# Performance work log

Hardware: AMD Instinct MI355X
Metric: run time of the kernel (lower is better)

## Reference

```python
import jax, jax.numpy as jnp
import numpy as np

EPS = 1e-6
TAU = 0.07


def setup_inputs() -> dict:
    key = jax.random.key(0)
    kx, ky = jax.random.split(key)
    B, D = 4096, 1024
    x = jax.random.normal(kx, (B, D), dtype=jnp.float32)
    y = jax.random.normal(ky, (B, D), dtype=jnp.float32)
    return {"x": x, "y": y}


def reference(x, y):
    B = x.shape[0]
    # torch CosineSimilarity: dot / (max(||x||, eps) * max(||y||, eps))
    xn = x / jnp.maximum(jnp.linalg.norm(x, axis=-1, keepdims=True), EPS)
    yn = y / jnp.maximum(jnp.linalg.norm(y, axis=-1, keepdims=True), EPS)
    S = jnp.einsum('id,jd->ij', xn, yn)          # [B, B] cosine sims, S[i,j]=cos(x_i,y_j)
    E = jnp.exp(S / TAU)                          # bounded: |S|<=1 so exp <= e^{1/0.07}
    diag = jnp.diagonal(E)
    # original: sum_j (exp + eps) + eps  ->  sum_j exp + B*eps + eps
    extra = B * EPS + EPS
    row_denom = jnp.sum(E, axis=1) + extra        # x->y direction (loop 1)
    col_denom = jnp.sum(E, axis=0) + extra        # y->x direction (loop 2)
    coef = -1.0 / (2.0 * B)
    loss = coef * (jnp.sum(jnp.log(diag / row_denom)) + jnp.sum(jnp.log(diag / col_denom)))
    return loss
```

## Files before the change

### kernel.cpp

```cpp
#include <hip/hip_runtime.h>
#include <hip/hip_bf16.h>

#define NB 4096
#define DK 1024
#define EPSF 1e-6f
#define QSCALE 16.0f

typedef __attribute__((ext_vector_type(8))) int   i32x8_t;
typedef __attribute__((ext_vector_type(4))) int   i32x4_t;
typedef __attribute__((ext_vector_type(4))) float f32x4_t;


__device__ __forceinline__ void async16(const void* g, void* lds) {
    __builtin_amdgcn_global_load_lds(
        (const __attribute__((address_space(1))) void*)g,
        (__attribute__((address_space(3))) void*)lds, 16, 0, 0);
}

__global__ __launch_bounds__(256) void normalize_rows(
    const float* __restrict__ x, const float* __restrict__ y,
    unsigned char* __restrict__ xq, unsigned char* __restrict__ yq,
    float* __restrict__ sdiag, float* __restrict__ zerobuf)
{
    const int t = threadIdx.x;
    const int gid = blockIdx.x * 256 + t;
    if (gid < 2 * NB) zerobuf[gid] = 0.f;

    const int wave = t >> 6;
    const int lane = t & 63;
    const int row  = blockIdx.x * 4 + wave;

    const float4* xr = reinterpret_cast<const float4*>(x + (size_t)row * DK);
    const float4* yr = reinterpret_cast<const float4*>(y + (size_t)row * DK);

    float4 xv[4], yv[4];
    float ssx = 0.f, ssy = 0.f, sxy = 0.f;
    #pragma unroll
    for (int jj = 0; jj < 4; ++jj) {
        xv[jj] = xr[lane * 4 + jj];
        yv[jj] = yr[lane * 4 + jj];
        ssx += xv[jj].x*xv[jj].x + xv[jj].y*xv[jj].y + xv[jj].z*xv[jj].z + xv[jj].w*xv[jj].w;
        ssy += yv[jj].x*yv[jj].x + yv[jj].y*yv[jj].y + yv[jj].z*yv[jj].z + yv[jj].w*yv[jj].w;
        sxy += xv[jj].x*yv[jj].x + xv[jj].y*yv[jj].y + xv[jj].z*yv[jj].z + xv[jj].w*yv[jj].w;
    }
    #pragma unroll
    for (int off = 1; off < 64; off <<= 1) {
        ssx += __shfl_xor(ssx, off, 64);
        ssy += __shfl_xor(ssy, off, 64);
        sxy += __shfl_xor(sxy, off, 64);
    }
    const float invx = 1.0f / fmaxf(sqrtf(ssx), EPSF);
    const float invy = 1.0f / fmaxf(sqrtf(ssy), EPSF);
    const float sx = invx * QSCALE;
    const float sy = invy * QSCALE;

    i32x4_t xb, yb;
    #pragma unroll
    for (int jj = 0; jj < 4; ++jj) {
        int px = __builtin_amdgcn_cvt_pk_fp8_f32(xv[jj].x * sx, xv[jj].y * sx, 0, false);
        px     = __builtin_amdgcn_cvt_pk_fp8_f32(xv[jj].z * sx, xv[jj].w * sx, px, true);
        int py = __builtin_amdgcn_cvt_pk_fp8_f32(yv[jj].x * sy, yv[jj].y * sy, 0, false);
        py     = __builtin_amdgcn_cvt_pk_fp8_f32(yv[jj].z * sy, yv[jj].w * sy, py, true);
        xb[jj] = px;
        yb[jj] = py;
    }

    const int p = row >> 4, r = row & 15;
    const unsigned off = (unsigned)(p * 32 + (lane >> 3) * 4) * 512
                       + r * 128 + ((((lane & 7) ^ (r & 7))) << 4);
    *reinterpret_cast<i32x4_t*>(xq + off) = xb;
    *reinterpret_cast<i32x4_t*>(yq + off) = yb;

    if (lane == 0) sdiag[row] = sxy * invx * invy;
}

__global__ __launch_bounds__(512) void gemm_exp_sums(
    const unsigned char* __restrict__ xq, const unsigned char* __restrict__ yq,
    float* __restrict__ rowsum, float* __restrict__ colsum)
{
    __shared__ __align__(16) unsigned char As[32 * 1024];
    __shared__ __align__(16) unsigned char Bs[32 * 1024];

    const int t    = threadIdx.x;
    const int lane = t & 63;
    const int wave = t >> 6;
    const int q    = lane >> 4;
    const int l15  = lane & 15;

    const int R0 = blockIdx.y * 256;
    const int C0 = blockIdx.x * 256;
    const int wRow = (wave >> 2) * 64;
    const int wCol = (wave & 3) * 64;

    f32x4_t acc[2][4][4];
    #pragma unroll
    for (int hh = 0; hh < 2; hh++)
        #pragma unroll
        for (int i = 0; i < 4; i++)
            #pragma unroll
            for (int j = 0; j < 4; j++)
                acc[hh][i][j] = (f32x4_t){0.f, 0.f, 0.f, 0.f};

    const unsigned char* srcA =
        xq + (size_t)((R0 >> 4) + wave) * 16384 + lane * 16;
    const unsigned char* srcB =
        yq + (size_t)((C0 >> 4) + wave) * 16384 + lane * 16;

    const int sLo = (((2 * q)    ) ^ (l15 & 7)) << 4;
    const int sHi = (((2 * q) + 1) ^ (l15 & 7)) << 4;

    #pragma unroll 1
    for (int kb = 0; kb < 8; ++kb) {
        __syncthreads();
        #pragma unroll
        for (int h2 = 0; h2 < 2; ++h2) {
            async16(srcA + kb * 2048 + h2 * 1024,          &As[wave * 2048 + h2 * 1024]);
            async16(srcA + kb * 2048 + h2 * 1024 + 131072, &As[(wave + 8) * 2048 + h2 * 1024]);
            async16(srcB + kb * 2048 + h2 * 1024,          &Bs[wave * 2048 + h2 * 1024]);
            async16(srcB + kb * 2048 + h2 * 1024 + 131072, &Bs[(wave + 8) * 2048 + h2 * 1024]);
        }
        __syncthreads();

        i32x8_t bfr[4];
        #pragma unroll
        for (int nt = 0; nt < 4; ++nt) {
            const unsigned char* c = &Bs[((wCol >> 4) + nt) * 2048 + l15 * 128];
            const i32x4_t lo = *reinterpret_cast<const i32x4_t*>(c + sLo);
            const i32x4_t hi = *reinterpret_cast<const i32x4_t*>(c + sHi);
            bfr[nt][0] = lo[0]; bfr[nt][1] = lo[1]; bfr[nt][2] = lo[2]; bfr[nt][3] = lo[3];
            bfr[nt][4] = hi[0]; bfr[nt][5] = hi[1]; bfr[nt][6] = hi[2]; bfr[nt][7] = hi[3];
        }
        #pragma unroll
        for (int hh = 0; hh < 2; ++hh) {
            #pragma unroll
            for (int mt = 0; mt < 4; ++mt) {
                const unsigned char* c =
                    &As[((wRow >> 4) + hh * 8 + mt) * 2048 + l15 * 128];
                const i32x4_t lo = *reinterpret_cast<const i32x4_t*>(c + sLo);
                const i32x4_t hi = *reinterpret_cast<const i32x4_t*>(c + sHi);
                i32x8_t af;
                af[0] = lo[0]; af[1] = lo[1]; af[2] = lo[2]; af[3] = lo[3];
                af[4] = hi[0]; af[5] = hi[1]; af[6] = hi[2]; af[7] = hi[3];
                #pragma unroll
                for (int nt = 0; nt < 4; ++nt)
                    acc[hh][mt][nt] = __builtin_amdgcn_mfma_scale_f32_16x16x128_f8f6f4(
                        af, bfr[nt], acc[hh][mt][nt],
                        0, 0,
                        0, 0x7F7F7F7F,
                        0, 0x7F7F7F7F);
            }
        }
    }

    const float kScale = (float)(1.0 / (256.0 * 0.07 * 0.6931471805599453));
    float csum[4] = {0.f, 0.f, 0.f, 0.f};
    #pragma unroll
    for (int hh = 0; hh < 2; ++hh) {
        #pragma unroll
        for (int mt = 0; mt < 4; ++mt) {
            float rsum[4] = {0.f, 0.f, 0.f, 0.f};
            #pragma unroll
            for (int nt = 0; nt < 4; ++nt) {
                #pragma unroll
                for (int r = 0; r < 4; ++r) {
                    const float e = exp2f(acc[hh][mt][nt][r] * kScale);
                    rsum[r]  += e;
                    csum[nt] += e;
                }
            }
            #pragma unroll
            for (int r = 0; r < 4; ++r) {
                float v = rsum[r];
                v += __shfl_xor(v, 1, 64);
                v += __shfl_xor(v, 2, 64);
                v += __shfl_xor(v, 4, 64);
                v += __shfl_xor(v, 8, 64);
                if (l15 == 0)
                    atomicAdd(&rowsum[R0 + wRow + hh * 128 + mt * 16 + q * 4 + r], v);
            }
        }
    }
    #pragma unroll
    for (int nt = 0; nt < 4; ++nt) {
        float v = csum[nt];
        v += __shfl_xor(v, 16, 64);
        v += __shfl_xor(v, 32, 64);
        if (lane < 16)
            atomicAdd(&colsum[C0 + wCol + nt * 16 + l15], v);
    }
}

__global__ __launch_bounds__(1024) void finalize(
    const float* __restrict__ rowsum, const float* __restrict__ colsum,
    const float* __restrict__ sdiag, float* __restrict__ out)
{
    const float extra = (float)(NB * 1e-6 + 1e-6);
    double local = 0.0;
    for (int i = threadIdx.x; i < NB; i += 1024) {
        local += (double)sdiag[i] * (2.0 / 0.07)
               - (double)logf(rowsum[i] + extra)
               - (double)logf(colsum[i] + extra);
    }
    #pragma unroll
    for (int off = 1; off < 64; off <<= 1)
        local += __shfl_xor(local, off, 64);
    __shared__ double dred[16];
    const int wave = threadIdx.x >> 6;
    if ((threadIdx.x & 63) == 0) dred[wave] = local;
    __syncthreads();
    if (threadIdx.x == 0) {
        double tot = 0.0;
        #pragma unroll
        for (int w = 0; w < 16; ++w) tot += dred[w];
        out[0] = (float)(tot * (-1.0 / (2.0 * NB)));
    }
}

extern "C" void kernel_launch(void* const* d_in, const int* in_sizes, int n_in,
                              void* d_out, int out_size, void* d_ws, size_t ws_size,
                              hipStream_t stream)
{
    const float* x = (const float*)d_in[0];
    const float* y = (const float*)d_in[1];
    float* out = (float*)d_out;

    char* ws = (char*)d_ws;
    unsigned char* xq = (unsigned char*)ws;
    unsigned char* yq = (unsigned char*)(ws + (size_t)4 * 1024 * 1024);
    float* rowsum = (float*)(ws + (size_t)8 * 1024 * 1024);
    float* colsum = rowsum + NB;
    float* sdiag  = colsum + NB;

    normalize_rows<<<NB / 4, 256, 0, stream>>>(x, y, xq, yq, sdiag, rowsum);

    dim3 grid(16, 16);
    gemm_exp_sums<<<grid, 512, 0, stream>>>(xq, yq, rowsum, colsum);

    finalize<<<1, 1024, 0, stream>>>(rowsum, colsum, sdiag, out);
}
```

Measured before the change: 107.4 us.

## Shrink GEMM tile to 128x128 and double-buffer LDS with async prefetch

The fused FP8 GEMM+exp kernel moves from 256x256 tiles with 512 threads to 128x128 tiles with 256 threads, so the grid grows from 256 to 1024 blocks. It also double-buffers shared memory, prefetching the next K slab with async global-to-LDS loads while the MFMAs run on the current one, synchronised by waitcnt and barriers. The aim is to fill all CUs better and hide load latency. In exchange, each tile reuses less data, so global traffic and atomic row/column updates go up.

```diff
diff --git a/kernel.cpp b/kernel.cpp
--- a/kernel.cpp
+++ b/kernel.cpp
@@ -74,12 +74,11 @@
     if (lane == 0) sdiag[row] = sxy * invx * invy;
 }
 
-__global__ __launch_bounds__(512) void gemm_exp_sums(
+__global__ __launch_bounds__(256) void gemm_exp_sums(
     const unsigned char* __restrict__ xq, const unsigned char* __restrict__ yq,
     float* __restrict__ rowsum, float* __restrict__ colsum)
 {
-    __shared__ __align__(16) unsigned char As[32 * 1024];
-    __shared__ __align__(16) unsigned char Bs[32 * 1024];
+    __shared__ __align__(16) unsigned char LDS[2][32768];
 
     const int t    = threadIdx.x;
     const int lane = t & 63;
@@ -87,97 +86,108 @@
     const int q    = lane >> 4;
     const int l15  = lane & 15;
 
-    const int R0 = blockIdx.y * 256;
-    const int C0 = blockIdx.x * 256;
-    const int wRow = (wave >> 2) * 64;
-    const int wCol = (wave & 3) * 64;
-
-    f32x4_t acc[2][4][4];
-    #pragma unroll
-    for (int hh = 0; hh < 2; hh++)
-        #pragma unroll
-        for (int i = 0; i < 4; i++)
-            #pragma unroll
-            for (int j = 0; j < 4; j++)
-                acc[hh][i][j] = (f32x4_t){0.f, 0.f, 0.f, 0.f};
+    const int R0 = blockIdx.y * 128;
+    const int C0 = blockIdx.x * 128;
+    const int wRow = (wave >> 1) * 64;
+    const int wCol = (wave & 1) * 64;
+
+    f32x4_t acc[4][4];
+    #pragma unroll
+    for (int i = 0; i < 4; i++)
+        #pragma unroll
+        for (int j = 0; j < 4; j++)
+            acc[i][j] = (f32x4_t){0.f, 0.f, 0.f, 0.f};
 
     const unsigned char* srcA =
-        xq + (size_t)((R0 >> 4) + wave) * 16384 + lane * 16;
+        xq + (size_t)((R0 >> 4) + 2 * wave) * 16384 + lane * 16;
     const unsigned char* srcB =
-        yq + (size_t)((C0 >> 4) + wave) * 16384 + lane * 16;
+        yq + (size_t)((C0 >> 4) + 2 * wave) * 16384 + lane * 16;
 
     const int sLo = (((2 * q)    ) ^ (l15 & 7)) << 4;
     const int sHi = (((2 * q) + 1) ^ (l15 & 7)) << 4;
 
+    auto issue = [&](int kb, int buf) {
+        unsigned char* base = &LDS[buf][0];
+        #pragma unroll
+        for (int pp = 0; pp < 2; ++pp) {
+            #pragma unroll
+            for (int h2 = 0; h2 < 2; ++h2) {
+                async16(srcA + pp * 16384 + kb * 2048 + h2 * 1024,
+                        base + (2 * wave + pp) * 2048 + h2 * 1024);
+                async16(srcB + pp * 16384 + kb * 2048 + h2 * 1024,
+                        base + 16384 + (2 * wave + pp) * 2048 + h2 * 1024);
+            }
+        }
+    };
+
+    issue(0, 0);
+
     #pragma unroll 1
     for (int kb = 0; kb < 8; ++kb) {
-        __syncthreads();
-        #pragma unroll
-        for (int h2 = 0; h2 < 2; ++h2) {
-            async16(srcA + kb * 2048 + h2 * 1024,          &As[wave * 2048 + h2 * 1024]);
-            async16(srcA + kb * 2048 + h2 * 1024 + 131072, &As[(wave + 8) * 2048 + h2 * 1024]);
-            async16(srcB + kb * 2048 + h2 * 1024,          &Bs[wave * 2048 + h2 * 1024]);
-            async16(srcB + kb * 2048 + h2 * 1024 + 131072, &Bs[(wave + 8) * 2048 + h2 * 1024]);
-        }
-        __syncthreads();
+        const int buf = kb & 1;
+        if (kb < 7) {
+            issue(kb + 1, buf ^ 1);
+            __builtin_amdgcn_s_waitcnt(0xF78);
+        } else {
+            __builtin_amdgcn_s_waitcnt(0xF70);
+        }
+        __builtin_amdgcn_s_barrier();
+
+        const unsigned char* Ab = &LDS[buf][0];
+        const unsigned char* Bb = &LDS[buf][16384];
 
         i32x8_t bfr[4];
         #pragma unroll
         for (int nt = 0; nt < 4; ++nt) {
-            const unsigned char* c = &Bs[((wCol >> 4) + nt) * 2048 + l15 * 128];
+            const unsigned char* c = Bb + ((wCol >> 4) + nt) * 2048 + l15 * 128;
             const i32x4_t lo = *reinterpret_cast<const i32x4_t*>(c + sLo);
             const i32x4_t hi = *reinterpret_cast<const i32x4_t*>(c + sHi);
             bfr[nt][0] = lo[0]; bfr[nt][1] = lo[1]; bfr[nt][2] = lo[2]; bfr[nt][3] = lo[3];
             bfr[nt][4] = hi[0]; bfr[nt][5] = hi[1]; bfr[nt][6] = hi[2]; bfr[nt][7] = hi[3];
         }
         #pragma unroll
-        for (int hh = 0; hh < 2; ++hh) {
+        for (int mt = 0; mt < 4; ++mt) {
+            const unsigned char* c = Ab + ((wRow >> 4) + mt) * 2048 + l15 * 128;
+            const i32x4_t lo = *reinterpret_cast<const i32x4_t*>(c + sLo);
+            const i32x4_t hi = *reinterpret_cast<const i32x4_t*>(c + sHi);
+            i32x8_t af;
+            af[0] = lo[0]; af[1] = lo[1]; af[2] = lo[2]; af[3] = lo[3];
+            af[4] = hi[0]; af[5] = hi[1]; af[6] = hi[2]; af[7] = hi[3];
             #pragma unroll
-            for (int mt = 0; mt < 4; ++mt) {
-                const unsigned char* c =
-                    &As[((wRow >> 4) + hh * 8 + mt) * 2048 + l15 * 128];
-                const i32x4_t lo = *reinterpret_cast<const i32x4_t*>(c + sLo);
-                const i32x4_t hi = *reinterpret_cast<const i32x4_t*>(c + sHi);
-                i32x8_t af;
-                af[0] = lo[0]; af[1] = lo[1]; af[2] = lo[2]; af[3] = lo[3];
-                af[4] = hi[0]; af[5] = hi[1]; af[6] = hi[2]; af[7] = hi[3];
-                #pragma unroll
-                for (int nt = 0; nt < 4; ++nt)
-                    acc[hh][mt][nt] = __builtin_amdgcn_mfma_scale_f32_16x16x128_f8f6f4(
-                        af, bfr[nt], acc[hh][mt][nt],
-                        0, 0,
-                        0, 0x7F7F7F7F,
-                        0, 0x7F7F7F7F);
-            }
-        }
+            for (int nt = 0; nt < 4; ++nt)
+                acc[mt][nt] = __builtin_amdgcn_mfma_scale_f32_16x16x128_f8f6f4(
+                    af, bfr[nt], acc[mt][nt],
+                    0, 0,
+                    0, 0x7F7F7F7F,
+                    0, 0x7F7F7F7F);
+        }
+
+        __builtin_amdgcn_s_barrier();
     }
 
     const float kScale = (float)(1.0 / (256.0 * 0.07 * 0.6931471805599453));
     float csum[4] = {0.f, 0.f, 0.f, 0.f};
     #pragma unroll
-    for (int hh = 0; hh < 2; ++hh) {
-        #pragma unroll
-        for (int mt = 0; mt < 4; ++mt) {
-            float rsum[4] = {0.f, 0.f, 0.f, 0.f};
-            #pragma unroll
-            for (int nt = 0; nt < 4; ++nt) {
-                #pragma unroll
-                for (int r = 0; r < 4; ++r) {
-                    const float e = exp2f(acc[hh][mt][nt][r] * kScale);
-                    rsum[r]  += e;
-                    csum[nt] += e;
-                }
-            }
+    for (int mt = 0; mt < 4; ++mt) {
+        float rsum[4] = {0.f, 0.f, 0.f, 0.f};
+        #pragma unroll
+        for (int nt = 0; nt < 4; ++nt) {
             #pragma unroll
             for (int r = 0; r < 4; ++r) {
-                float v = rsum[r];
-                v += __shfl_xor(v, 1, 64);
-                v += __shfl_xor(v, 2, 64);
-                v += __shfl_xor(v, 4, 64);
-                v += __shfl_xor(v, 8, 64);
-                if (l15 == 0)
-                    atomicAdd(&rowsum[R0 + wRow + hh * 128 + mt * 16 + q * 4 + r], v);
+                const float e = exp2f(acc[mt][nt][r] * kScale);
+                rsum[r]  += e;
+                csum[nt] += e;
             }
+        }
+        #pragma unroll
+        for (int r = 0; r < 4; ++r) {
+            float v = rsum[r];
+            v += __shfl_xor(v, 1, 64);
+            v += __shfl_xor(v, 2, 64);
+            v += __shfl_xor(v, 4, 64);
+            v += __shfl_xor(v, 8, 64);
+            if (l15 == 0)
+                atomicAdd(&rowsum[R0 + wRow + mt * 16 + q * 4 + r], v);
         }
     }
     #pragma unroll
@@ -233,8 +243,8 @@
 
     normalize_rows<<<NB / 4, 256, 0, stream>>>(x, y, xq, yq, sdiag, rowsum);
 
-    dim3 grid(16, 16);
-    gemm_exp_sums<<<grid, 512, 0, stream>>>(xq, yq, rowsum, colsum);
+    dim3 grid(NB / 128, NB / 128);
+    gemm_exp_sums<<<grid, 256, 0, stream>>>(xq, yq, rowsum, colsum);
 
     finalize<<<1, 1024, 0, stream>>>(rowsum, colsum, sdiag, out);
 }
```

After: 111.7 us. 4.0% more time.

## Double-buffer LDS tiles to overlap next k-block loads with MFMA compute

Applied to the files above, without the earlier changes.

Replaces the single-buffered As/Bs staging with two 64 KB LDS buffers. The next k-block's async global-to-LDS loads are issued before computing on the current buffer, with explicit vmcnt waits and barriers in place of the two __syncthreads per iteration. The goal is to hide global load latency behind the FP8 MFMA work. The cost is doubling LDS to 128 KB per block, which may lower occupancy, and a manual waitcnt encoding that has to be correct on this target.

```diff
diff --git a/kernel.cpp b/kernel.cpp
--- a/kernel.cpp
+++ b/kernel.cpp
@@ -78,8 +78,7 @@
     const unsigned char* __restrict__ xq, const unsigned char* __restrict__ yq,
     float* __restrict__ rowsum, float* __restrict__ colsum)
 {
-    __shared__ __align__(16) unsigned char As[32 * 1024];
-    __shared__ __align__(16) unsigned char Bs[32 * 1024];
+    __shared__ __align__(16) unsigned char LDS[2][65536];
 
     const int t    = threadIdx.x;
     const int lane = t & 63;
@@ -102,29 +101,44 @@
                 acc[hh][i][j] = (f32x4_t){0.f, 0.f, 0.f, 0.f};
 
     const unsigned char* srcA =
-        xq + (size_t)((R0 >> 4) + wave) * 16384 + lane * 16;
+        xq + (size_t)((R0 >> 4) + 2 * wave) * 16384 + lane * 16;
     const unsigned char* srcB =
-        yq + (size_t)((C0 >> 4) + wave) * 16384 + lane * 16;
+        yq + (size_t)((C0 >> 4) + 2 * wave) * 16384 + lane * 16;
 
     const int sLo = (((2 * q)    ) ^ (l15 & 7)) << 4;
     const int sHi = (((2 * q) + 1) ^ (l15 & 7)) << 4;
 
+    auto issue = [&](int kb, int buf) {
+        #pragma unroll
+        for (int pp = 0; pp < 2; ++pp) {
+            #pragma unroll
+            for (int h2 = 0; h2 < 2; ++h2) {
+                async16(srcA + pp * 16384 + kb * 2048 + h2 * 1024,
+                        &LDS[buf][(2 * wave + pp) * 2048 + h2 * 1024]);
+                async16(srcB + pp * 16384 + kb * 2048 + h2 * 1024,
+                        &LDS[buf][32768 + (2 * wave + pp) * 2048 + h2 * 1024]);
+            }
+        }
+    };
+
+    issue(0, 0);
+
     #pragma unroll 1
     for (int kb = 0; kb < 8; ++kb) {
-        __syncthreads();
-        #pragma unroll
-        for (int h2 = 0; h2 < 2; ++h2) {
-            async16(srcA + kb * 2048 + h2 * 1024,          &As[wave * 2048 + h2 * 1024]);
-            async16(srcA + kb * 2048 + h2 * 1024 + 131072, &As[(wave + 8) * 2048 + h2 * 1024]);
-            async16(srcB + kb * 2048 + h2 * 1024,          &Bs[wave * 2048 + h2 * 1024]);
-            async16(srcB + kb * 2048 + h2 * 1024 + 131072, &Bs[(wave + 8) * 2048 + h2 * 1024]);
-        }
-        __syncthreads();
+        const int buf = kb & 1;
+        if (kb < 7) {
+            issue(kb + 1, buf ^ 1);
+            __builtin_amdgcn_s_waitcnt(0xF78);
+        } else {
+            __builtin_amdgcn_s_waitcnt(0xF70);
+        }
+        __builtin_amdgcn_s_barrier();
 
         i32x8_t bfr[4];
         #pragma unroll
         for (int nt = 0; nt < 4; ++nt) {
-            const unsigned char* c = &Bs[((wCol >> 4) + nt) * 2048 + l15 * 128];
+            const unsigned char* c =
+                &LDS[buf][32768 + ((wCol >> 4) + nt) * 2048 + l15 * 128];
             const i32x4_t lo = *reinterpret_cast<const i32x4_t*>(c + sLo);
             const i32x4_t hi = *reinterpret_cast<const i32x4_t*>(c + sHi);
             bfr[nt][0] = lo[0]; bfr[nt][1] = lo[1]; bfr[nt][2] = lo[2]; bfr[nt][3] = lo[3];
@@ -135,7 +149,7 @@
             #pragma unroll
             for (int mt = 0; mt < 4; ++mt) {
                 const unsigned char* c =
-                    &As[((wRow >> 4) + hh * 8 + mt) * 2048 + l15 * 128];
+                    &LDS[buf][((wRow >> 4) + hh * 8 + mt) * 2048 + l15 * 128];
                 const i32x4_t lo = *reinterpret_cast<const i32x4_t*>(c + sLo);
                 const i32x4_t hi = *reinterpret_cast<const i32x4_t*>(c + sHi);
                 i32x8_t af;
@@ -150,6 +164,8 @@
                         0, 0x7F7F7F7F);
             }
         }
+
+        __builtin_amdgcn_s_barrier();
     }
 
     const float kScale = (float)(1.0 / (256.0 * 0.07 * 0.6931471805599453));
```

After: 103.9 us. 1.03x faster.
